# Kernel tuning notes

Hardware: AMD Instinct MI355X
Metric: run time of the kernel (lower is better)

## Reference

```python
import jax, jax.numpy as jnp
import numpy as np

N, E = 10000, 320000
NF, HF = 256, 256  # input_nf/output_nf, hidden_nf
EPS = 1e-8


def setup_inputs() -> dict:
    key = jax.random.key(0)
    ks = jax.random.split(key, 20)
    h = jax.random.normal(ks[0], (N, NF), jnp.float32)
    coord = jax.random.normal(ks[1], (N, 3), jnp.float32)
    edge_index = jax.random.randint(ks[2], (2, E), 0, N, jnp.int32)

    def dense(k, fan_in, fan_out, scale=None):
        s = scale if scale is not None else 1.0 / np.sqrt(fan_in)
        W = jax.random.normal(k, (fan_in, fan_out), jnp.float32) * s
        b = jnp.zeros((fan_out,), jnp.float32)
        return W, b

    We1, be1 = dense(ks[3], 2 * NF + 1, HF)   # edge_mlp layer 1
    We2, be2 = dense(ks[4], HF, HF)           # edge_mlp layer 2
    Wn1, bn1 = dense(ks[5], HF + NF, HF)      # node_mlp layer 1
    Wn2, bn2 = dense(ks[6], HF, NF)           # node_mlp layer 2
    Wc1, bc1 = dense(ks[7], HF, HF)           # coord_mlp layer 1
    Wc2, bc2 = dense(ks[8], HF, 1, scale=0.001)  # coord_mlp final, tiny init (xavier gain=0.001)
    return dict(h=h, coord=coord, edge_index=edge_index,
                We1=We1, be1=be1, We2=We2, be2=be2,
                Wn1=Wn1, bn1=bn1, Wn2=Wn2, bn2=bn2,
                Wc1=Wc1, bc1=bc1, Wc2=Wc2, bc2=bc2)


def _segment_sum(data, seg_ids, num_segments):
    return jax.ops.segment_sum(data, seg_ids, num_segments=num_segments)


def reference(h, coord, edge_index, We1, be1, We2, be2, Wn1, bn1, Wn2, bn2, Wc1, bc1, Wc2, bc2):
    row, col = edge_index[0], edge_index[1]

    # coord2radial
    coord_diff = coord[row] - coord[col]                    # [E, 3]
    radial = jnp.sum(coord_diff ** 2, axis=1, keepdims=True)  # [E, 1]

    # edge model: MLP on [h_i, h_j, ||x_i - x_j||^2]
    edge_in = jnp.concatenate([h[row], h[col], radial], axis=1)  # [E, 2*NF+1]
    e = jax.nn.silu(edge_in @ We1 + be1)
    edge_feat = jax.nn.silu(e @ We2 + be2)                  # [E, HF]

    # coord model: coord_diff * coord_mlp(edge_feat), mean-aggregated
    c = jax.nn.silu(edge_feat @ Wc1 + bc1)
    trans = coord_diff * (c @ Wc2 + bc2)                    # [E, 3]
    agg_c = _segment_sum(trans, row, coord.shape[0])
    count = _segment_sum(jnp.ones_like(trans), row, coord.shape[0])
    coord_out = coord + agg_c / jnp.clip(count, 1.0)

    # node model: sum-aggregate edge features, concat with h, MLP
    agg_h = _segment_sum(edge_feat, row, h.shape[0])        # [N, HF]
    node_in = jnp.concatenate([h, agg_h], axis=1)           # [N, HF+NF]
    n = jax.nn.silu(node_in @ Wn1 + bn1)
    h_out = n @ Wn2 + bn2                                   # [N, NF]

    return h_out, coord_out
```

## Files before the change

kernel.cpp:

```cpp
#include <hip/hip_runtime.h>
#include <hip/hip_bf16.h>

typedef __bf16 bf16;
typedef __attribute__((ext_vector_type(8))) __bf16 bf16x8;
typedef __attribute__((ext_vector_type(4))) float f32x4;

static_assert(sizeof(bf16x8) == 16, "bf16x8 must be 16B");

constexpr int N_NODES = 10000;
constexpr int N_EDGES = 320000;
constexpr int KPAD    = 264;

__device__ __forceinline__ float silu_f(float x) { return x / (1.0f + __expf(-x)); }

__device__ __forceinline__ unsigned pk_bf16(float lo, float hi) {
  unsigned a = __float_as_uint(lo) + 0x8000u;
  unsigned b = __float_as_uint(hi) + 0x8000u;
  return __builtin_amdgcn_perm(b, a, 0x07060302u);
}

__device__ __forceinline__ void mfmaT_k256(const bf16* __restrict__ WT, int wstride, int koff,
                                           const bf16* Albs, int w, int r, int q, f32x4 acc[4][4]) {
  for (int k0 = 0; k0 < 256; k0 += 32) {
    bf16x8 a[4], b[4];
#pragma unroll
    for (int mi = 0; mi < 4; ++mi)
      a[mi] = *(const bf16x8*)(WT + (size_t)(w * 64 + 16 * mi + r) * wstride + koff + k0 + q * 8);
#pragma unroll
    for (int ni = 0; ni < 4; ++ni)
      b[ni] = *(const bf16x8*)(Albs + (16 * ni + r) * KPAD + k0 + q * 8);
#pragma unroll
    for (int mi = 0; mi < 4; ++mi)
#pragma unroll
      for (int ni = 0; ni < 4; ++ni)
        acc[mi][ni] = __builtin_amdgcn_mfma_f32_16x16x32_bf16(a[mi], b[ni], acc[mi][ni], 0, 0, 0);
  }
}

__global__ __launch_bounds__(256) void prep_kernel(
    const float* __restrict__ h, const float* __restrict__ We1, const float* __restrict__ We2,
    const float* __restrict__ Wn1, const float* __restrict__ Wn2, const float* __restrict__ Wc1,
    const int* __restrict__ eidx,
    bf16* __restrict__ Hb, bf16* __restrict__ We1T, bf16* __restrict__ Wn1T,
    bf16* __restrict__ We2T, bf16* __restrict__ Wn2T, bf16* __restrict__ Wc1T,
    int* __restrict__ hist) {
  int bid = blockIdx.x, tid = threadIdx.x;
  if (bid < 10000) { int i = bid * 256 + tid; Hb[i] = (bf16)h[i]; return; }
  if (bid >= 11792) {
    int e = (bid - 11792) * 256 + tid;
    if (e < N_EDGES) atomicAdd(&hist[eidx[e]], 1);
    return;
  }
  int t = (bid - 10000) * 256 + tid;
  if (t < 131072) { int k = t >> 8, j = t & 255; We1T[j * 512 + k] = (bf16)We1[k * 256 + j]; return; }
  t -= 131072;
  if (t < 131072) { int k = t >> 8, j = t & 255; Wn1T[j * 512 + k] = (bf16)Wn1[k * 256 + j]; return; }
  t -= 131072;
  if (t < 65536) { int k = t >> 8, j = t & 255; We2T[j * 256 + k] = (bf16)We2[k * 256 + j]; return; }
  t -= 65536;
  if (t < 65536) { int k = t >> 8, j = t & 255; Wn2T[j * 256 + k] = (bf16)Wn2[k * 256 + j]; return; }
  t -= 65536;
  if (t < 65536) { int k = t >> 8, j = t & 255; Wc1T[j * 256 + k] = (bf16)Wc1[k * 256 + j]; return; }
}

__global__ __launch_bounds__(256) void scan_kernel(const int* __restrict__ hist,
                                                   int* __restrict__ base, int* __restrict__ cursor) {
  __shared__ int partial[256];
  int t = threadIdx.x;
  int s = 0;
  for (int i = 0; i < 40; ++i) { int idx = t * 40 + i; if (idx < N_NODES) s += hist[idx]; }
  partial[t] = s;
  __syncthreads();
  for (int d = 1; d < 256; d <<= 1) {
    int v = (t >= d) ? partial[t - d] : 0;
    __syncthreads();
    partial[t] += v;
    __syncthreads();
  }
  int run = partial[t] - s;
  for (int i = 0; i < 40; ++i) {
    int idx = t * 40 + i;
    if (idx < N_NODES) { base[idx] = run; cursor[idx] = run; run += hist[idx]; }
  }
}

__global__ __launch_bounds__(256) void scatter_kernel(const int* __restrict__ eidx, int* __restrict__ cursor,
                                                      int* __restrict__ rs, int* __restrict__ cs) {
  int e = blockIdx.x * 256 + threadIdx.x;
  if (e < N_EDGES) {
    int r = eidx[e], c = eidx[N_EDGES + e];
    int p = atomicAdd(&cursor[r], 1);
    rs[p] = r; cs[p] = c;
  }
}

__global__ __launch_bounds__(256, 2) void gemm_pq(const bf16* __restrict__ Hb,
                                                  const bf16* __restrict__ We1T,
                                                  const float* __restrict__ be1,
                                                  bf16* __restrict__ P, bf16* __restrict__ Q) {
  int tid = threadIdx.x, w = tid >> 6, lane = tid & 63, r = lane & 15, q = lane >> 4;
  int m0 = blockIdx.x * 64;
  int koff = blockIdx.y ? 256 : 0;
  bf16* OUT = blockIdx.y ? Q : P;
  bool addb = (blockIdx.y == 0);
  f32x4 acc[4][4];
#pragma unroll
  for (int mi = 0; mi < 4; ++mi)
#pragma unroll
    for (int ni = 0; ni < 4; ++ni) acc[mi][ni] = (f32x4){0.f, 0.f, 0.f, 0.f};

  for (int k0 = 0; k0 < 256; k0 += 32) {
    bf16x8 a[4], b[4];
#pragma unroll
    for (int mi = 0; mi < 4; ++mi)
      a[mi] = *(const bf16x8*)(We1T + (size_t)(w * 64 + 16 * mi + r) * 512 + koff + k0 + q * 8);
#pragma unroll
    for (int ni = 0; ni < 4; ++ni) {
      int m = m0 + 16 * ni + r; if (m > N_NODES - 1) m = N_NODES - 1;
      b[ni] = *(const bf16x8*)(Hb + (size_t)m * 256 + k0 + q * 8);
    }
#pragma unroll
    for (int mi = 0; mi < 4; ++mi)
#pragma unroll
      for (int ni = 0; ni < 4; ++ni)
        acc[mi][ni] = __builtin_amdgcn_mfma_f32_16x16x32_bf16(a[mi], b[ni], acc[mi][ni], 0, 0, 0);
  }
#pragma unroll
  for (int mi = 0; mi < 4; ++mi) {
    int ch = w * 64 + 16 * mi + 4 * q;
    float4 bv = addb ? *(const float4*)(be1 + ch) : (float4){0.f, 0.f, 0.f, 0.f};
#pragma unroll
    for (int ni = 0; ni < 4; ++ni) {
      int m = m0 + 16 * ni + r;
      if (m < N_NODES) {
        uint2 o;
        o.x = pk_bf16(acc[mi][ni][0] + bv.x, acc[mi][ni][1] + bv.y);
        o.y = pk_bf16(acc[mi][ni][2] + bv.z, acc[mi][ni][3] + bv.w);
        *(uint2*)(OUT + (size_t)m * 256 + ch) = o;
      }
    }
  }
}

__global__ __launch_bounds__(256, 4) void edge_kernel(
    const float* __restrict__ coord, const int* __restrict__ rs, const int* __restrict__ cs,
    const float* __restrict__ We1,
    const float* __restrict__ be2, const float* __restrict__ bc1,
    const float* __restrict__ Wc2, const float* __restrict__ bc2,
    const bf16* __restrict__ P, const bf16* __restrict__ Q,
    const bf16* __restrict__ We2T, const bf16* __restrict__ Wc1T,
    float* __restrict__ agg_h, float* __restrict__ agg_c) {
  __shared__ __align__(16) bf16 buf[64 * KPAD];
  __shared__ int s_row[64], s_col[64];
  __shared__ float s_rad[64], s_cd[64][3], s_part[64][4], s_scal[64];
  __shared__ int s_rs[65];
  __shared__ int s_nrun;

  int tid = threadIdx.x;
  int e0 = blockIdx.x * 64;
  int w = tid >> 6, lane = tid & 63, r = lane & 15, q = lane >> 4;

  if (tid < 64) {
    int e = e0 + tid;
    int ri = rs[e], ci = cs[e];
    s_row[tid] = ri; s_col[tid] = ci;
    float dx = coord[3 * ri + 0] - coord[3 * ci + 0];
    float dy = coord[3 * ri + 1] - coord[3 * ci + 1];
    float dz = coord[3 * ri + 2] - coord[3 * ci + 2];
    s_cd[tid][0] = dx; s_cd[tid][1] = dy; s_cd[tid][2] = dz;
    s_rad[tid] = dx * dx + dy * dy + dz * dz;
  }
  __syncthreads();

  if (tid < 64) {
    bool bnd = (tid == 0) || (s_row[tid] != s_row[tid - 1]);
    unsigned long long m = __ballot(bnd);
    int rank = __popcll(m & ((1ull << tid) - 1ull));
    if (bnd) s_rs[rank] = tid;
    if (tid == 0) { int R = __popcll(m); s_nrun = R; s_rs[R] = 64; }
  }

  {
    int off = (tid & 31) * 8;
    int esub = tid >> 5;
    float4 wa = *(const float4*)(We1 + 512 * 256 + off);
    float4 wb = *(const float4*)(We1 + 512 * 256 + off + 4);
#pragma unroll
    for (int p = 0; p < 8; ++p) {
      int e = p * 8 + esub;
      int ri = s_row[e], ci = s_col[e];
      bf16x8 pv = *(const bf16x8*)(P + (size_t)ri * 256 + off);
      bf16x8 qv = *(const bf16x8*)(Q + (size_t)ci * 256 + off);
      float rad = s_rad[e];
      float f0 = silu_f((float)pv[0] + (float)qv[0] + rad * wa.x);
      float f1 = silu_f((float)pv[1] + (float)qv[1] + rad * wa.y);
      float f2 = silu_f((float)pv[2] + (float)qv[2] + rad * wa.z);
      float f3 = silu_f((float)pv[3] + (float)qv[3] + rad * wa.w);
      float f4 = silu_f((float)pv[4] + (float)qv[4] + rad * wb.x);
      float f5 = silu_f((float)pv[5] + (float)qv[5] + rad * wb.y);
      float f6 = silu_f((float)pv[6] + (float)qv[6] + rad * wb.z);
      float f7 = silu_f((float)pv[7] + (float)qv[7] + rad * wb.w);
      uint4 o;
      o.x = pk_bf16(f0, f1); o.y = pk_bf16(f2, f3);
      o.z = pk_bf16(f4, f5); o.w = pk_bf16(f6, f7);
      *(uint4*)(buf + e * KPAD + off) = o;
    }
  }
  __syncthreads();

  {
    f32x4 acc[4][4];
#pragma unroll
    for (int mi = 0; mi < 4; ++mi)
#pragma unroll
      for (int ni = 0; ni < 4; ++ni) acc[mi][ni] = (f32x4){0.f, 0.f, 0.f, 0.f};
    mfmaT_k256(We2T, 256, 0, buf, w, r, q, acc);
    __syncthreads();
#pragma unroll
    for (int mi = 0; mi < 4; ++mi) {
      int ch = w * 64 + 16 * mi + 4 * q;
      float4 bv = *(const float4*)(be2 + ch);
#pragma unroll
      for (int ni = 0; ni < 4; ++ni) {
        int edge = 16 * ni + r;
        float f0 = silu_f(acc[mi][ni][0] + bv.x);
        float f1 = silu_f(acc[mi][ni][1] + bv.y);
        float f2 = silu_f(acc[mi][ni][2] + bv.z);
        float f3 = silu_f(acc[mi][ni][3] + bv.w);
        uint2 o; o.x = pk_bf16(f0, f1); o.y = pk_bf16(f2, f3);
        *(uint2*)(buf + edge * KPAD + ch) = o;
      }
    }
  }
  __syncthreads();

  f32x4 acc2[4][4];
#pragma unroll
  for (int mi = 0; mi < 4; ++mi)
#pragma unroll
    for (int ni = 0; ni < 4; ++ni) acc2[mi][ni] = (f32x4){0.f, 0.f, 0.f, 0.f};
  mfmaT_k256(Wc1T, 256, 0, buf, w, r, q, acc2);

  {
    int R = s_nrun;
    for (int rr = 0; rr < R; ++rr) {
      int st = s_rs[rr], en = s_rs[rr + 1];
      float s = 0.f;
      for (int e = st; e < en; ++e) s += (float)buf[e * KPAD + tid];
      atomicAdd(&agg_h[(size_t)s_row[st] * 256 + tid], s);
    }
  }
  __syncthreads();

#pragma unroll
  for (int mi = 0; mi < 4; ++mi) {
    int ch = w * 64 + 16 * mi + 4 * q;
    float4 bv = *(const float4*)(bc1 + ch);
#pragma unroll
    for (int ni = 0; ni < 4; ++ni) {
      int edge = 16 * ni + r;
      float f0 = silu_f(acc2[mi][ni][0] + bv.x);
      float f1 = silu_f(acc2[mi][ni][1] + bv.y);
      float f2 = silu_f(acc2[mi][ni][2] + bv.z);
      float f3 = silu_f(acc2[mi][ni][3] + bv.w);
      uint2 o; o.x = pk_bf16(f0, f1); o.y = pk_bf16(f2, f3);
      *(uint2*)(buf + edge * KPAD + ch) = o;
    }
  }
  __syncthreads();

  {
    int e = tid >> 2, p = tid & 3;
    float s = 0.f;
#pragma unroll
    for (int kk = 0; kk < 64; kk += 8) {
      bf16x8 v = *(const bf16x8*)(buf + e * KPAD + p * 64 + kk);
      float4 w0 = *(const float4*)(Wc2 + p * 64 + kk);
      float4 w1 = *(const float4*)(Wc2 + p * 64 + kk + 4);
      s += (float)v[0] * w0.x + (float)v[1] * w0.y + (float)v[2] * w0.z + (float)v[3] * w0.w
         + (float)v[4] * w1.x + (float)v[5] * w1.y + (float)v[6] * w1.z + (float)v[7] * w1.w;
    }
    s_part[e][p] = s;
  }
  __syncthreads();
  if (tid < 64)
    s_scal[tid] = s_part[tid][0] + s_part[tid][1] + s_part[tid][2] + s_part[tid][3] + bc2[0];
  __syncthreads();

  if (tid < 3) {
    int R = s_nrun;
    for (int rr = 0; rr < R; ++rr) {
      int st = s_rs[rr], en = s_rs[rr + 1];
      float s = 0.f;
      for (int e = st; e < en; ++e) s += s_cd[e][tid] * s_scal[e];
      atomicAdd(&agg_c[3 * s_row[st] + tid], s);
    }
  }
}

__global__ __launch_bounds__(256, 2) void node_kernel(
    const bf16* __restrict__ Hb, const float* __restrict__ agg_h,
    const int* __restrict__ hist, const float* __restrict__ coord, const float* __restrict__ agg_c,
    const bf16* __restrict__ Wn1T, const bf16* __restrict__ Wn2T,
    const float* __restrict__ bn1, const float* __restrict__ bn2,
    float* __restrict__ h_out, float* __restrict__ coord_out) {
  __shared__ __align__(16) bf16 buf[64 * KPAD];
  int tid = threadIdx.x, w = tid >> 6, lane = tid & 63, r = lane & 15, q = lane >> 4;
  int m0 = blockIdx.x * 64;

  if (tid < 64) {
    int m = m0 + tid;
    if (m < N_NODES) {
      float c = (float)hist[m]; if (c < 1.f) c = 1.f;
      coord_out[3 * m + 0] = coord[3 * m + 0] + agg_c[3 * m + 0] / c;
      coord_out[3 * m + 1] = coord[3 * m + 1] + agg_c[3 * m + 1] / c;
      coord_out[3 * m + 2] = coord[3 * m + 2] + agg_c[3 * m + 2] / c;
    }
  }

  f32x4 acc[4][4];
#pragma unroll
  for (int mi = 0; mi < 4; ++mi)
#pragma unroll
    for (int ni = 0; ni < 4; ++ni) acc[mi][ni] = (f32x4){0.f, 0.f, 0.f, 0.f};
  for (int k0 = 0; k0 < 256; k0 += 32) {
    bf16x8 a[4], b[4];
#pragma unroll
    for (int mi = 0; mi < 4; ++mi)
      a[mi] = *(const bf16x8*)(Wn1T + (size_t)(w * 64 + 16 * mi + r) * 512 + k0 + q * 8);
#pragma unroll
    for (int ni = 0; ni < 4; ++ni) {
      int m = m0 + 16 * ni + r; if (m > N_NODES - 1) m = N_NODES - 1;
      b[ni] = *(const bf16x8*)(Hb + (size_t)m * 256 + k0 + q * 8);
    }
#pragma unroll
    for (int mi = 0; mi < 4; ++mi)
#pragma unroll
      for (int ni = 0; ni < 4; ++ni)
        acc[mi][ni] = __builtin_amdgcn_mfma_f32_16x16x32_bf16(a[mi], b[ni], acc[mi][ni], 0, 0, 0);
  }
  for (int k0 = 0; k0 < 256; k0 += 32) {
    bf16x8 a[4], b[4];
#pragma unroll
    for (int mi = 0; mi < 4; ++mi)
      a[mi] = *(const bf16x8*)(Wn1T + (size_t)(w * 64 + 16 * mi + r) * 512 + 256 + k0 + q * 8);
#pragma unroll
    for (int ni = 0; ni < 4; ++ni) {
      int m = m0 + 16 * ni + r; if (m > N_NODES - 1) m = N_NODES - 1;
      const float* ap = agg_h + (size_t)m * 256 + k0 + q * 8;
      float4 u = *(const float4*)ap;
      float4 v = *(const float4*)(ap + 4);
      uint4 o;
      o.x = pk_bf16(u.x, u.y); o.y = pk_bf16(u.z, u.w);
      o.z = pk_bf16(v.x, v.y); o.w = pk_bf16(v.z, v.w);
      b[ni] = *(const bf16x8*)&o;
    }
#pragma unroll
    for (int mi = 0; mi < 4; ++mi)
#pragma unroll
      for (int ni = 0; ni < 4; ++ni)
        acc[mi][ni] = __builtin_amdgcn_mfma_f32_16x16x32_bf16(a[mi], b[ni], acc[mi][ni], 0, 0, 0);
  }
  __syncthreads();
#pragma unroll
  for (int mi = 0; mi < 4; ++mi) {
    int ch = w * 64 + 16 * mi + 4 * q;
    float4 bv = *(const float4*)(bn1 + ch);
#pragma unroll
    for (int ni = 0; ni < 4; ++ni) {
      int lm = 16 * ni + r;
      float f0 = silu_f(acc[mi][ni][0] + bv.x);
      float f1 = silu_f(acc[mi][ni][1] + bv.y);
      float f2 = silu_f(acc[mi][ni][2] + bv.z);
      float f3 = silu_f(acc[mi][ni][3] + bv.w);
      uint2 o; o.x = pk_bf16(f0, f1); o.y = pk_bf16(f2, f3);
      *(uint2*)(buf + lm * KPAD + ch) = o;
    }
  }
  __syncthreads();
  f32x4 acc2[4][4];
#pragma unroll
  for (int mi = 0; mi < 4; ++mi)
#pragma unroll
    for (int ni = 0; ni < 4; ++ni) acc2[mi][ni] = (f32x4){0.f, 0.f, 0.f, 0.f};
  mfmaT_k256(Wn2T, 256, 0, buf, w, r, q, acc2);
#pragma unroll
  for (int mi = 0; mi < 4; ++mi) {
    int ch = w * 64 + 16 * mi + 4 * q;
    float4 bv = *(const float4*)(bn2 + ch);
#pragma unroll
    for (int ni = 0; ni < 4; ++ni) {
      int m = m0 + 16 * ni + r;
      if (m < N_NODES) {
        float4 o;
        o.x = acc2[mi][ni][0] + bv.x;
        o.y = acc2[mi][ni][1] + bv.y;
        o.z = acc2[mi][ni][2] + bv.z;
        o.w = acc2[mi][ni][3] + bv.w;
        *(float4*)(h_out + (size_t)m * 256 + ch) = o;
      }
    }
  }
}

extern "C" void kernel_launch(void* const* d_in, const int* in_sizes, int n_in,
                              void* d_out, int out_size, void* d_ws, size_t ws_size,
                              hipStream_t stream) {
  const float* h     = (const float*)d_in[0];
  const float* coord = (const float*)d_in[1];
  const int*   eidx  = (const int*)d_in[2];
  const float* We1 = (const float*)d_in[3];
  const float* be1 = (const float*)d_in[4];
  const float* We2 = (const float*)d_in[5];
  const float* be2 = (const float*)d_in[6];
  const float* Wn1 = (const float*)d_in[7];
  const float* bn1 = (const float*)d_in[8];
  const float* Wn2 = (const float*)d_in[9];
  const float* bn2 = (const float*)d_in[10];
  const float* Wc1 = (const float*)d_in[11];
  const float* bc1 = (const float*)d_in[12];
  const float* Wc2 = (const float*)d_in[13];
  const float* bc2 = (const float*)d_in[14];

  char* ws = (char*)d_ws;
  float* agg_h = (float*)(ws + 0);
  float* agg_c = (float*)(ws + 10240000);
  int*   hist  = (int*)  (ws + 10360000);
  int*   base  = (int*)  (ws + 10400000);
  int*   cursor= (int*)  (ws + 10440000);
  int*   rs    = (int*)  (ws + 10480000);
  int*   cs    = (int*)  (ws + 11760000);
  bf16* Hb   = (bf16*)(ws + 13040000);
  bf16* P    = (bf16*)(ws + 18160000);
  bf16* Q    = (bf16*)(ws + 23280000);
  bf16* We1T = (bf16*)(ws + 28400000);
  bf16* Wn1T = (bf16*)(ws + 28662144);
  bf16* We2T = (bf16*)(ws + 28924288);
  bf16* Wn2T = (bf16*)(ws + 29055360);
  bf16* Wc1T = (bf16*)(ws + 29186432);

  float* h_out = (float*)d_out;
  float* coord_out = h_out + (size_t)N_NODES * 256;

  hipMemsetAsync(ws, 0, 10400000, stream);
  prep_kernel<<<13042, 256, 0, stream>>>(h, We1, We2, Wn1, Wn2, Wc1, eidx,
                                         Hb, We1T, Wn1T, We2T, Wn2T, Wc1T, hist);
  scan_kernel<<<1, 256, 0, stream>>>(hist, base, cursor);
  scatter_kernel<<<1250, 256, 0, stream>>>(eidx, cursor, rs, cs);
  gemm_pq<<<dim3(157, 2), 256, 0, stream>>>(Hb, We1T, be1, P, Q);
  edge_kernel<<<5000, 256, 0, stream>>>(coord, rs, cs, We1, be2, bc1, Wc2, bc2,
                                        P, Q, We2T, Wc1T, agg_h, agg_c);
  node_kernel<<<157, 256, 0, stream>>>(Hb, agg_h, hist, coord, agg_c,
                                       Wn1T, Wn2T, bn1, bn2, h_out, coord_out);
}
```

Measured before the change: 463.1 us.

## Split edge kernel work across 8 waves per 64-edge block

New measurement: 607.4 us. +31.2%, slower.

```diff
diff --git a/kernel.cpp b/kernel.cpp
--- a/kernel.cpp
+++ b/kernel.cpp
@@ -33,6 +33,25 @@
     for (int mi = 0; mi < 4; ++mi)
 #pragma unroll
       for (int ni = 0; ni < 4; ++ni)
+        acc[mi][ni] = __builtin_amdgcn_mfma_f32_16x16x32_bf16(a[mi], b[ni], acc[mi][ni], 0, 0, 0);
+  }
+}
+
+__device__ __forceinline__ void mfmaT_k256_8w(const bf16* __restrict__ WT, int wstride,
+                                              const bf16* Albs, int wch, int weh, int r, int q,
+                                              f32x4 acc[4][2]) {
+  for (int k0 = 0; k0 < 256; k0 += 32) {
+    bf16x8 a[4], b[2];
+#pragma unroll
+    for (int ni = 0; ni < 2; ++ni)
+      b[ni] = *(const bf16x8*)(Albs + (weh * 32 + 16 * ni + r) * KPAD + k0 + q * 8);
+#pragma unroll
+    for (int mi = 0; mi < 4; ++mi)
+      a[mi] = *(const bf16x8*)(WT + (size_t)(wch * 64 + 16 * mi + r) * wstride + k0 + q * 8);
+#pragma unroll
+    for (int mi = 0; mi < 4; ++mi)
+#pragma unroll
+      for (int ni = 0; ni < 2; ++ni)
         acc[mi][ni] = __builtin_amdgcn_mfma_f32_16x16x32_bf16(a[mi], b[ni], acc[mi][ni], 0, 0, 0);
   }
 }
@@ -142,7 +161,7 @@
   }
 }
 
-__global__ __launch_bounds__(256, 4) void edge_kernel(
+__global__ __launch_bounds__(512, 8) void edge_kernel(
     const float* __restrict__ coord, const int* __restrict__ rs, const int* __restrict__ cs,
     const float* __restrict__ We1,
     const float* __restrict__ be2, const float* __restrict__ bc1,
@@ -152,13 +171,14 @@
     float* __restrict__ agg_h, float* __restrict__ agg_c) {
   __shared__ __align__(16) bf16 buf[64 * KPAD];
   __shared__ int s_row[64], s_col[64];
-  __shared__ float s_rad[64], s_cd[64][3], s_part[64][4], s_scal[64];
+  __shared__ float s_rad[64], s_cd[64][3], s_part[64][8], s_scal[64];
   __shared__ int s_rs[65];
   __shared__ int s_nrun;
 
   int tid = threadIdx.x;
   int e0 = blockIdx.x * 64;
   int w = tid >> 6, lane = tid & 63, r = lane & 15, q = lane >> 4;
+  int wch = w & 3, weh = w >> 2;
 
   if (tid < 64) {
     int e = e0 + tid;
@@ -186,8 +206,8 @@
     float4 wa = *(const float4*)(We1 + 512 * 256 + off);
     float4 wb = *(const float4*)(We1 + 512 * 256 + off + 4);
 #pragma unroll
-    for (int p = 0; p < 8; ++p) {
-      int e = p * 8 + esub;
+    for (int p = 0; p < 4; ++p) {
+      int e = p * 16 + esub;
       int ri = s_row[e], ci = s_col[e];
       bf16x8 pv = *(const bf16x8*)(P + (size_t)ri * 256 + off);
       bf16x8 qv = *(const bf16x8*)(Q + (size_t)ci * 256 + off);
@@ -209,20 +229,20 @@
   __syncthreads();
 
   {
-    f32x4 acc[4][4];
-#pragma unroll
-    for (int mi = 0; mi < 4; ++mi)
-#pragma unroll
-      for (int ni = 0; ni < 4; ++ni) acc[mi][ni] = (f32x4){0.f, 0.f, 0.f, 0.f};
-    mfmaT_k256(We2T, 256, 0, buf, w, r, q, acc);
+    f32x4 acc[4][2];
+#pragma unroll
+    for (int mi = 0; mi < 4; ++mi)
+#pragma unroll
+      for (int ni = 0; ni < 2; ++ni) acc[mi][ni] = (f32x4){0.f, 0.f, 0.f, 0.f};
+    mfmaT_k256_8w(We2T, 256, buf, wch, weh, r, q, acc);
     __syncthreads();
 #pragma unroll
     for (int mi = 0; mi < 4; ++mi) {
-      int ch = w * 64 + 16 * mi + 4 * q;
+      int ch = wch * 64 + 16 * mi + 4 * q;
       float4 bv = *(const float4*)(be2 + ch);
 #pragma unroll
-      for (int ni = 0; ni < 4; ++ni) {
-        int edge = 16 * ni + r;
+      for (int ni = 0; ni < 2; ++ni) {
+        int edge = weh * 32 + 16 * ni + r;
         float f0 = silu_f(acc[mi][ni][0] + bv.x);
         float f1 = silu_f(acc[mi][ni][1] + bv.y);
         float f2 = silu_f(acc[mi][ni][2] + bv.z);
@@ -234,31 +254,32 @@
   }
   __syncthreads();
 
-  f32x4 acc2[4][4];
+  f32x4 acc2[4][2];
 #pragma unroll
   for (int mi = 0; mi < 4; ++mi)
 #pragma unroll
-    for (int ni = 0; ni < 4; ++ni) acc2[mi][ni] = (f32x4){0.f, 0.f, 0.f, 0.f};
-  mfmaT_k256(Wc1T, 256, 0, buf, w, r, q, acc2);
+    for (int ni = 0; ni < 2; ++ni) acc2[mi][ni] = (f32x4){0.f, 0.f, 0.f, 0.f};
+  mfmaT_k256_8w(Wc1T, 256, buf, wch, weh, r, q, acc2);
 
   {
     int R = s_nrun;
-    for (int rr = 0; rr < R; ++rr) {
+    int ch = tid & 255, g = tid >> 8;
+    for (int rr = g; rr < R; rr += 2) {
       int st = s_rs[rr], en = s_rs[rr + 1];
       float s = 0.f;
-      for (int e = st; e < en; ++e) s += (float)buf[e * KPAD + tid];
-      atomicAdd(&agg_h[(size_t)s_row[st] * 256 + tid], s);
+      for (int e = st; e < en; ++e) s += (float)buf[e * KPAD + ch];
+      atomicAdd(&agg_h[(size_t)s_row[st] * 256 + ch], s);
     }
   }
   __syncthreads();
 
 #pragma unroll
   for (int mi = 0; mi < 4; ++mi) {
-    int ch = w * 64 + 16 * mi + 4 * q;
+    int ch = wch * 64 + 16 * mi + 4 * q;
     float4 bv = *(const float4*)(bc1 + ch);
 #pragma unroll
-    for (int ni = 0; ni < 4; ++ni) {
-      int edge = 16 * ni + r;
+    for (int ni = 0; ni < 2; ++ni) {
+      int edge = weh * 32 + 16 * ni + r;
       float f0 = silu_f(acc2[mi][ni][0] + bv.x);
       float f1 = silu_f(acc2[mi][ni][1] + bv.y);
       float f2 = silu_f(acc2[mi][ni][2] + bv.z);
@@ -270,21 +291,25 @@
   __syncthreads();
 
   {
-    int e = tid >> 2, p = tid & 3;
+    int e = tid >> 3, p = tid & 7;
     float s = 0.f;
 #pragma unroll
-    for (int kk = 0; kk < 64; kk += 8) {
-      bf16x8 v = *(const bf16x8*)(buf + e * KPAD + p * 64 + kk);
-      float4 w0 = *(const float4*)(Wc2 + p * 64 + kk);
-      float4 w1 = *(const float4*)(Wc2 + p * 64 + kk + 4);
+    for (int kk = 0; kk < 32; kk += 8) {
+      bf16x8 v = *(const bf16x8*)(buf + e * KPAD + p * 32 + kk);
+      float4 w0 = *(const float4*)(Wc2 + p * 32 + kk);
+      float4 w1 = *(const float4*)(Wc2 + p * 32 + kk + 4);
       s += (float)v[0] * w0.x + (float)v[1] * w0.y + (float)v[2] * w0.z + (float)v[3] * w0.w
          + (float)v[4] * w1.x + (float)v[5] * w1.y + (float)v[6] * w1.z + (float)v[7] * w1.w;
     }
     s_part[e][p] = s;
   }
   __syncthreads();
-  if (tid < 64)
-    s_scal[tid] = s_part[tid][0] + s_part[tid][1] + s_part[tid][2] + s_part[tid][3] + bc2[0];
+  if (tid < 64) {
+    float s = 0.f;
+#pragma unroll
+    for (int p = 0; p < 8; ++p) s += s_part[tid][p];
+    s_scal[tid] = s + bc2[0];
+  }
   __syncthreads();
 
   if (tid < 3) {
@@ -448,7 +473,7 @@
   scan_kernel<<<1, 256, 0, stream>>>(hist, base, cursor);
   scatter_kernel<<<1250, 256, 0, stream>>>(eidx, cursor, rs, cs);
   gemm_pq<<<dim3(157, 2), 256, 0, stream>>>(Hb, We1T, be1, P, Q);
-  edge_kernel<<<5000, 256, 0, stream>>>(coord, rs, cs, We1, be2, bc1, Wc2, bc2,
+  edge_kernel<<<5000, 512, 0, stream>>>(coord, rs, cs, We1, be2, bc1, Wc2, bc2,
                                         P, Q, We2T, Wc1T, agg_h, agg_c);
   node_kernel<<<157, 256, 0, stream>>>(Hb, agg_h, hist, coord, agg_c,
                                        Wn1T, Wn2T, bn1, bn2, h_out, coord_out);
```
